# Optimization experiments

Hardware: AMD Instinct MI355X
Metric: run time of the kernel (lower is better)

## Reference

```python
import jax, jax.numpy as jnp
import numpy as np

N = 50000       # nodes
E = 800000      # edges (before self loops)
DIN = 128       # input feature width
H = 4           # heads
C = 64          # hidden width per head
NCLS = 2        # num classes
NEG_SLOPE = 0.2 # PyG GATConv default negative_slope


def setup_inputs() -> dict:
    key = jax.random.key(0)
    ks = jax.random.split(key, 16)
    x = jax.random.normal(ks[0], (N, DIN), dtype=jnp.float32)
    edge_index = jax.random.randint(ks[1], (2, E), 0, N, dtype=jnp.int64)
    s = 0.05
    # layer 0: DIN -> H*C
    W0 = jax.random.normal(ks[2], (DIN, H * C), dtype=jnp.float32) * s
    a_src0 = jax.random.normal(ks[3], (H, C), dtype=jnp.float32) * s
    a_dst0 = jax.random.normal(ks[4], (H, C), dtype=jnp.float32) * s
    b0 = jnp.zeros((H * C,), dtype=jnp.float32)
    # layer 1: H*C -> H*C
    W1 = jax.random.normal(ks[5], (H * C, H * C), dtype=jnp.float32) * s
    a_src1 = jax.random.normal(ks[6], (H, C), dtype=jnp.float32) * s
    a_dst1 = jax.random.normal(ks[7], (H, C), dtype=jnp.float32) * s
    b1 = jnp.zeros((H * C,), dtype=jnp.float32)
    # layer 2: H*C -> NCLS, single head
    W2 = jax.random.normal(ks[8], (H * C, NCLS), dtype=jnp.float32) * s
    a_src2 = jax.random.normal(ks[9], (1, NCLS), dtype=jnp.float32) * s
    a_dst2 = jax.random.normal(ks[10], (1, NCLS), dtype=jnp.float32) * s
    b2 = jnp.zeros((NCLS,), dtype=jnp.float32)
    return {"x": x, "edge_index": edge_index,
            "W0": W0, "a_src0": a_src0, "a_dst0": a_dst0, "b0": b0,
            "W1": W1, "a_src1": a_src1, "a_dst1": a_dst1, "b1": b1,
            "W2": W2, "a_src2": a_src2, "a_dst2": a_dst2, "b2": b2}


def gat_conv(x, ei, W, a_src, a_dst, b, heads, out_c):
    """PyG-style GATConv (add_self_loops already applied to ei, concat=True)."""
    n = x.shape[0]
    h = (x @ W).reshape(n, heads, out_c)              # [N, H, C]
    src, dst = ei[0], ei[1]
    asrc = (h * a_src).sum(-1)                         # [N, H]
    adst = (h * a_dst).sum(-1)                         # [N, H]
    alpha = jax.nn.leaky_relu(asrc[src] + adst[dst], NEG_SLOPE)  # [E', H]
    # segment softmax over incoming edges of each dst node
    amax = jax.ops.segment_max(alpha, dst, num_segments=n)        # [N, H]
    e = jnp.exp(alpha - amax[dst])
    denom = jax.ops.segment_sum(e, dst, num_segments=n)
    coef = e / denom[dst]                              # [E', H]
    msg = h[src] * coef[:, :, None]                    # [E', H, C]
    out = jax.ops.segment_sum(msg, dst, num_segments=n)           # [N, H, C]
    return out.reshape(n, heads * out_c) + b


def reference(x, edge_index, W0, a_src0, a_dst0, b0,
              W1, a_src1, a_dst1, b1, W2, a_src2, a_dst2, b2):
    # Inference mode: dropout(p=0.5, training=False) is identity.
    loops = jnp.arange(N, dtype=edge_index.dtype)
    ei = jnp.concatenate([edge_index, jnp.stack([loops, loops])], axis=1)
    h = jnp.tanh(gat_conv(x, ei, W0, a_src0, a_dst0, b0, H, C))
    h = jnp.tanh(gat_conv(h, ei, W1, a_src1, a_dst1, b1, H, C))
    h = gat_conv(h, ei, W2, a_src2, a_dst2, b2, 1, NCLS)
    return jax.nn.softmax(h, axis=1), h
```

## Files before the change

### kernel.cpp

```cpp
#include <hip/hip_runtime.h>

#define NEG 0.2f

typedef float f32x4 __attribute__((ext_vector_type(4)));
typedef short bf16x8 __attribute__((ext_vector_type(8)));

struct __align__(8) us4 { unsigned short v[4]; };
struct __align__(16) us8 { unsigned short v[8]; };

__device__ __forceinline__ float b2f(unsigned short u){
  union { unsigned int i; float f; } x; x.i = ((unsigned int)u) << 16; return x.f;
}
__device__ __forceinline__ unsigned short f2b(float f){
  union { float f; unsigned int i; } x; x.f = f;
  unsigned int r = x.i + 0x7FFFu + ((x.i >> 16) & 1u);
  return (unsigned short)(r >> 16);
}


__global__ void k_pack_w(const float* __restrict__ W, unsigned short* __restrict__ Wp, int K){
  int t = blockIdx.x*blockDim.x + threadIdx.x;
  int KB = K >> 5;
  if (t >= 16*KB*64) return;
  int lane = t & 63;
  int nb = (t >> 6) & 15;
  int kb = (t >> 6) >> 4;
  int kbase = kb*32 + ((lane>>4)<<3);
  int col = nb*16 + (lane&15);
  #pragma unroll
  for (int j=0;j<8;j++) Wp[(size_t)t*8 + j] = f2b(W[(size_t)(kbase+j)*256 + col]);
}

__global__ void k_detect(const int* __restrict__ ei, int* __restrict__ meta){
  if (blockIdx.x==0 && threadIdx.x==0){
    int o = 0;
    #pragma unroll
    for (int j=1;j<128;j+=2) o |= ei[j];
    meta[0] = (o==0) ? 1 : 0;
  }
}

__global__ void k_deg(const int* __restrict__ ei, const int* __restrict__ meta,
                      int* __restrict__ deg, int E, int EP, int N){
  int e = blockIdx.x*blockDim.x + threadIdx.x;
  if (e >= EP) return;
  int s, d;
  if (e < E){
    if (meta[0]){ s = ei[2*(size_t)e]; d = ei[2*(size_t)(E+e)]; }
    else        { s = ei[e];           d = ei[E+e]; }
  } else { s = d = e - E; }
  if ((unsigned)d >= (unsigned)N || (unsigned)s >= (unsigned)N) return;
  atomicAdd(deg + d, 1);
}

__global__ void k_scan1(const int* __restrict__ deg, int* __restrict__ tmp,
                        int* __restrict__ bsum, int N){
  __shared__ int s[256];
  int t = threadIdx.x;
  int i = blockIdx.x*256 + t;
  int v = (i < N) ? deg[i] : 0;
  s[t] = v;
  __syncthreads();
  for (int off=1; off<256; off<<=1){
    int x = (t>=off) ? s[t-off] : 0;
    __syncthreads();
    s[t] += x;
    __syncthreads();
  }
  if (i < N) tmp[i] = s[t] - v;
  if (t == 255) bsum[blockIdx.x] = s[255];
}

__global__ void k_scan2(const int* __restrict__ bsum, int* __restrict__ bsumx,
                        int* __restrict__ meta, int n){
  __shared__ int s[256];
  int t = threadIdx.x;
  int v = (t < n) ? bsum[t] : 0;
  s[t] = v;
  __syncthreads();
  for (int off=1; off<256; off<<=1){
    int x = (t>=off) ? s[t-off] : 0;
    __syncthreads();
    s[t] += x;
    __syncthreads();
  }
  bsumx[t] = s[t] - v;
  if (t == 255) meta[1] = s[255];
}

__global__ void k_scan3(const int* __restrict__ tmp, const int* __restrict__ bsumx,
                        const int* __restrict__ meta,
                        int* __restrict__ rp, int* __restrict__ cur, int N){
  int i = blockIdx.x*256 + threadIdx.x;
  if (i < N){ int v = tmp[i] + bsumx[i>>8]; rp[i] = v; cur[i] = v; }
  if (i == 0) rp[N] = meta[1];
}

__global__ void k_fill(const int* __restrict__ ei, const int* __restrict__ meta,
                       int* __restrict__ cur, int* __restrict__ csr, int E, int EP, int N){
  int e = blockIdx.x*blockDim.x + threadIdx.x;
  if (e >= EP) return;
  int s, d;
  if (e < E){
    if (meta[0]){ s = ei[2*(size_t)e]; d = ei[2*(size_t)(E+e)]; }
    else        { s = ei[e];           d = ei[E+e]; }
  } else { s = d = e - E; }
  if ((unsigned)d >= (unsigned)N || (unsigned)s >= (unsigned)N) return;
  int pos = atomicAdd(cur + d, 1);
  csr[pos] = s;
}

template<int K, int CVT>
__global__ __launch_bounds__(256) void k_gemm(const void* __restrict__ Xv,
    const unsigned short* __restrict__ Wp,
    const float* __restrict__ aS, const float* __restrict__ aD,
    unsigned short* __restrict__ Hout,
    float* __restrict__ asrc, float* __restrict__ adst, int N){
  constexpr int KB = K/32;
  __shared__ short sB[2][16*64*8];
  const int lane = threadIdx.x & 63;
  const int wave = threadIdx.x >> 6;
  const int rowbase = blockIdx.x*64 + wave*16;
  const int l15 = lane & 15, lhi = lane >> 4;
  const int arow = rowbase + l15;

  bf16x8 aF[KB];
  if (CVT){
    const float* X = (const float*)Xv;
    #pragma unroll
    for (int kb=0; kb<KB; kb++){
      bf16x8 a = {};
      if (arow < N){
        f32x4 v0 = *(const f32x4*)(X + (size_t)arow*K + kb*32 + lhi*8);
        f32x4 v1 = *(const f32x4*)(X + (size_t)arow*K + kb*32 + lhi*8 + 4);
        #pragma unroll
        for (int j=0;j<4;j++){ a[j] = (short)f2b(v0[j]); a[j+4] = (short)f2b(v1[j]); }
      }
      aF[kb] = a;
    }
  } else {
    const unsigned short* X = (const unsigned short*)Xv;
    #pragma unroll
    for (int kb=0; kb<KB; kb++){
      bf16x8 a = {};
      if (arow < N) a = *(const bf16x8*)(X + (size_t)arow*K + kb*32 + lhi*8);
      aF[kb] = a;
    }
  }

  auto stage = [&](int buf, int kb){
    #pragma unroll
    for (int q=0;q<4;q++){
      int nb = wave*4 + q;
      const unsigned short* gsrc = Wp + ((size_t)((kb*16 + nb)*64) + lane)*8;
      __builtin_amdgcn_global_load_lds(
          (const __attribute__((address_space(1))) void*)gsrc,
          (__attribute__((address_space(3))) void*)&sB[buf][(size_t)nb*64*8],
          16, 0, 0);
    }
  };

  f32x4 acc[16] = {};
  stage(0, 0);
  __syncthreads();
  #pragma unroll
  for (int kb=0; kb<KB; kb++){
    const int cur = kb & 1;
    if (kb+1 < KB) stage(cur^1, kb+1);
    #pragma unroll
    for (int nb=0; nb<16; nb++){
      bf16x8 b = *(const bf16x8*)(&sB[cur][((size_t)nb*64 + lane)*8]);
      acc[nb] = __builtin_amdgcn_mfma_f32_16x16x32_bf16(aF[kb], b, acc[nb], 0, 0, 0);
    }
    __syncthreads();
  }

  const int r0 = rowbase + lhi*4;

  float sp[4][4] = {}; float dp[4][4] = {};
  #pragma unroll
  for (int h=0; h<4; h++){
    #pragma unroll
    for (int q=0; q<4; q++){
      const int nb = h*4 + q;
      float ws = aS[h*64 + q*16 + l15];
      float wd = aD[h*64 + q*16 + l15];
      #pragma unroll
      for (int r=0;r<4;r++){ sp[r][h] += acc[nb][r]*ws; dp[r][h] += acc[nb][r]*wd; }
    }
  }
  #pragma unroll
  for (int m=1;m<16;m<<=1){
    #pragma unroll
    for (int r=0;r<4;r++){
      #pragma unroll
      for (int h=0;h<4;h++){
        sp[r][h] += __shfl_xor(sp[r][h], m);
        dp[r][h] += __shfl_xor(dp[r][h], m);
      }
    }
  }
  if (l15 < 4){
    const int h = l15;
    #pragma unroll
    for (int r=0;r<4;r++){
      int row = r0 + r;
      if (row < N){ asrc[row*4+h] = sp[r][h]; adst[row*4+h] = dp[r][h]; }
    }
  }
  #pragma unroll
  for (int nb=0;nb<16;nb++){
    #pragma unroll
    for (int r=0;r<4;r++){
      int row = r0 + r;
      if (row < N) Hout[(size_t)row*256 + nb*16 + l15] = f2b(acc[nb][r]);
    }
  }
}

__global__ __launch_bounds__(256) void k_agg(const unsigned short* __restrict__ Hb,
    const float* __restrict__ asrc, const float* __restrict__ adst,
    const int* __restrict__ rp, const int* __restrict__ csr,
    const float* __restrict__ bias, unsigned short* __restrict__ Xout, int N){
  const int lane = threadIdx.x & 63;
  const int dst = blockIdx.x*4 + (threadIdx.x >> 6);
  if (dst >= N) return;
  const int head = lane >> 4;
  const int c0 = lane*4;
  const float ad = adst[dst*4 + head];
  const int s0 = rp[dst], s1 = rp[dst+1];
  float a0=0.f,a1=0.f,a2=0.f,a3=0.f,den=0.f;
  int e = s0;
  for (; e+4 <= s1; e += 4){
    int i0 = csr[e+0], i1 = csr[e+1], i2 = csr[e+2], i3 = csr[e+3];
    float x0 = asrc[(size_t)i0*4 + head];
    float x1 = asrc[(size_t)i1*4 + head];
    float x2 = asrc[(size_t)i2*4 + head];
    float x3 = asrc[(size_t)i3*4 + head];
    us4 h0 = *(const us4*)(Hb + (size_t)i0*256 + c0);
    us4 h1 = *(const us4*)(Hb + (size_t)i1*256 + c0);
    us4 h2 = *(const us4*)(Hb + (size_t)i2*256 + c0);
    us4 h3 = *(const us4*)(Hb + (size_t)i3*256 + c0);
    x0 += ad; x0 = x0 > 0.f ? x0 : NEG*x0; float e0 = __expf(x0);
    x1 += ad; x1 = x1 > 0.f ? x1 : NEG*x1; float e1 = __expf(x1);
    x2 += ad; x2 = x2 > 0.f ? x2 : NEG*x2; float e2 = __expf(x2);
    x3 += ad; x3 = x3 > 0.f ? x3 : NEG*x3; float e3 = __expf(x3);
    den += (e0 + e1) + (e2 + e3);
    a0 += e0*b2f(h0.v[0]) + e1*b2f(h1.v[0]) + e2*b2f(h2.v[0]) + e3*b2f(h3.v[0]);
    a1 += e0*b2f(h0.v[1]) + e1*b2f(h1.v[1]) + e2*b2f(h2.v[1]) + e3*b2f(h3.v[1]);
    a2 += e0*b2f(h0.v[2]) + e1*b2f(h1.v[2]) + e2*b2f(h2.v[2]) + e3*b2f(h3.v[2]);
    a3 += e0*b2f(h0.v[3]) + e1*b2f(h1.v[3]) + e2*b2f(h2.v[3]) + e3*b2f(h3.v[3]);
  }
  for (; e < s1; e++){
    int src = csr[e];
    float al = asrc[(size_t)src*4 + head] + ad;
    al = al > 0.f ? al : NEG*al;
    float ee = __expf(al);
    den += ee;
    us4 hv = *(const us4*)(Hb + (size_t)src*256 + c0);
    a0 += ee * b2f(hv.v[0]);
    a1 += ee * b2f(hv.v[1]);
    a2 += ee * b2f(hv.v[2]);
    a3 += ee * b2f(hv.v[3]);
  }
  float rd = 1.0f/den;
  us4 o;
  o.v[0] = f2b(tanhf(a0*rd + bias[c0+0]));
  o.v[1] = f2b(tanhf(a1*rd + bias[c0+1]));
  o.v[2] = f2b(tanhf(a2*rd + bias[c0+2]));
  o.v[3] = f2b(tanhf(a3*rd + bias[c0+3]));
  *(us4*)(Xout + (size_t)dst*256 + c0) = o;
}

__global__ __launch_bounds__(256) void k_gemm2(const unsigned short* __restrict__ X,
    const float* __restrict__ W2, const float* __restrict__ as2, const float* __restrict__ ad2,
    float* __restrict__ H2, float* __restrict__ asrc2, float* __restrict__ adst2, int N){
  __shared__ float sW[512];
  const int t = threadIdx.x;
  sW[t] = W2[t]; sW[t+256] = W2[t+256];
  __syncthreads();
  const int row = blockIdx.x*16 + (t>>4);
  const int sub = t & 15;
  float a0=0.f, a1=0.f;
  if (row < N){
    const unsigned short* xp = X + (size_t)row*256 + sub*16;
    #pragma unroll
    for (int jj=0;jj<4;jj++){
      us4 hv = *(const us4*)(xp + jj*4);
      #pragma unroll
      for (int j=0;j<4;j++){
        float f = b2f(hv.v[j]);
        int k = sub*16 + jj*4 + j;
        a0 += f * sW[k*2+0];
        a1 += f * sW[k*2+1];
      }
    }
  }
  #pragma unroll
  for (int m=1;m<16;m<<=1){ a0 += __shfl_xor(a0,m); a1 += __shfl_xor(a1,m); }
  if (sub==0 && row<N){
    H2[row*2+0]=a0; H2[row*2+1]=a1;
    asrc2[row] = a0*as2[0] + a1*as2[1];
    adst2[row] = a0*ad2[0] + a1*ad2[1];
  }
}

__global__ __launch_bounds__(256) void k_agg2(const float* __restrict__ H2,
    const float* __restrict__ asrc2, const float* __restrict__ adst2,
    const int* __restrict__ rp, const int* __restrict__ csr, const float* __restrict__ bb,
    float* __restrict__ out, int N){
  const int lane = threadIdx.x & 63;
  const int dst = blockIdx.x*4 + (threadIdx.x >> 6);
  if (dst >= N) return;
  const float ad = adst2[dst];
  const int s0 = rp[dst], s1 = rp[dst+1];
  float n0=0.f, n1=0.f, den=0.f;
  for (int e=s0+lane; e<s1; e+=64){
    int src = csr[e];
    float al = asrc2[src] + ad;
    al = al>0.f ? al : NEG*al;
    float ee = __expf(al);
    den += ee;
    n0 += ee * H2[src*2+0];
    n1 += ee * H2[src*2+1];
  }
  #pragma unroll
  for (int m=1;m<64;m<<=1){
    n0 += __shfl_xor(n0,m); n1 += __shfl_xor(n1,m); den += __shfl_xor(den,m);
  }
  if (lane==0){
    float o0 = n0/den + bb[0];
    float o1 = n1/den + bb[1];
    float mx = fmaxf(o0,o1);
    float e0 = __expf(o0-mx), e1 = __expf(o1-mx);
    float is = 1.0f/(e0+e1);
    out[(size_t)dst*2+0] = e0*is;
    out[(size_t)dst*2+1] = e1*is;
    out[(size_t)2*N + dst*2+0] = o0;
    out[(size_t)2*N + dst*2+1] = o1;
  }
}

extern "C" void kernel_launch(void* const* d_in, const int* in_sizes, int n_in,
                              void* d_out, int out_size, void* d_ws, size_t ws_size,
                              hipStream_t stream){
  const float* x  = (const float*)d_in[0];
  const int*   ei = (const int*)d_in[1];
  const float* W0 = (const float*)d_in[2];
  const float* as0= (const float*)d_in[3];
  const float* ad0= (const float*)d_in[4];
  const float* b0 = (const float*)d_in[5];
  const float* W1 = (const float*)d_in[6];
  const float* as1= (const float*)d_in[7];
  const float* ad1= (const float*)d_in[8];
  const float* b1 = (const float*)d_in[9];
  const float* W2 = (const float*)d_in[10];
  const float* as2= (const float*)d_in[11];
  const float* ad2= (const float*)d_in[12];
  const float* b2 = (const float*)d_in[13];

  const int N  = in_sizes[0] / 128;
  const int E  = in_sizes[1] / 2;
  const int EP = E + N;
  float* outp = (float*)d_out;

  char* w = (char*)d_ws;
  size_t off = 0;
  auto alloc = [&](size_t bytes)->char*{
    char* p = w + off; off = (off + bytes + 255) & ~(size_t)255; return p;
  };
  unsigned short* hb  = (unsigned short*)alloc((size_t)N*256*2);
  unsigned short* xa  = (unsigned short*)alloc((size_t)N*256*2);
  float* asrc  = (float*)alloc((size_t)N*4*4);
  float* adst  = (float*)alloc((size_t)N*4*4);
  float* asrc2 = (float*)alloc((size_t)N*4);
  float* adst2 = (float*)alloc((size_t)N*4);
  float* H2    = (float*)alloc((size_t)N*2*4);
  unsigned short* Wp0 = (unsigned short*)alloc((size_t)128*256*2);
  unsigned short* Wp1 = (unsigned short*)alloc((size_t)256*256*2);
  int* deg   = (int*)alloc((size_t)N*4);
  int* rp    = (int*)alloc((size_t)(N+1)*4);
  int* cur   = (int*)alloc((size_t)N*4);
  int* tmp   = (int*)alloc((size_t)N*4);
  int* bsum  = (int*)alloc(256*4);
  int* bsumx = (int*)alloc(256*4);
  int* meta  = (int*)alloc(8*4);
  int* csr   = (int*)alloc((size_t)EP*4);
  (void)ws_size; (void)n_in; (void)out_size;

  hipMemsetAsync(deg, 0, (size_t)N*4, stream);

  k_pack_w<<<(16*(128/32)*64 + 255)/256, 256, 0, stream>>>(W0, Wp0, 128);
  k_pack_w<<<(16*(256/32)*64 + 255)/256, 256, 0, stream>>>(W1, Wp1, 256);
  k_detect<<<1, 64, 0, stream>>>(ei, meta);
  k_deg   <<<(EP + 255)/256, 256, 0, stream>>>(ei, meta, deg, E, EP, N);
  const int nb1 = (N + 255)/256;
  k_scan1 <<<nb1, 256, 0, stream>>>(deg, tmp, bsum, N);
  k_scan2 <<<1, 256, 0, stream>>>(bsum, bsumx, meta, nb1);
  k_scan3 <<<nb1, 256, 0, stream>>>(tmp, bsumx, meta, rp, cur, N);
  k_fill  <<<(EP + 255)/256, 256, 0, stream>>>(ei, meta, cur, csr, E, EP, N);

  k_gemm<128,1><<<(N + 63)/64, 256, 0, stream>>>(x, Wp0, as0, ad0, hb, asrc, adst, N);
  k_agg        <<<(N + 3)/4, 256, 0, stream>>>(hb, asrc, adst, rp, csr, b0, xa, N);
  k_gemm<256,0><<<(N + 63)/64, 256, 0, stream>>>(xa, Wp1, as1, ad1, hb, asrc, adst, N);
  k_agg        <<<(N + 3)/4, 256, 0, stream>>>(hb, asrc, adst, rp, csr, b1, xa, N);
  k_gemm2      <<<(N + 15)/16, 256, 0, stream>>>(xa, W2, as2, ad2, H2, asrc2, adst2, N);
  k_agg2       <<<(N + 3)/4, 256, 0, stream>>>(H2, asrc2, adst2, rp, csr, b2, outp, N);
}
```

Measured before the change: 322.9 us.

## Merge setup launches, unroll aggregation by 8, use 16 lanes per node in agg2

Merges the memset and detect step into one init kernel and packs both weight matrices in a single launch, which cuts launch count. The main aggregation loop now handles 8 edges per step, putting more independent gathers in flight. The final aggregation gives each destination 16 lanes instead of a full 64-lane wavefront, since average degree is only about 17. The costs are higher register pressure in k_agg and slightly more complex code.

Result: faster. 311.6 us (-3.5%).

```diff
diff --git a/kernel.cpp b/kernel.cpp
--- a/kernel.cpp
+++ b/kernel.cpp
@@ -6,7 +6,6 @@
 typedef short bf16x8 __attribute__((ext_vector_type(8)));
 
 struct __align__(8) us4 { unsigned short v[4]; };
-struct __align__(16) us8 { unsigned short v[8]; };
 
 __device__ __forceinline__ float b2f(unsigned short u){
   union { unsigned int i; float f; } x; x.i = ((unsigned int)u) << 16; return x.f;
@@ -18,10 +17,15 @@
 }
 
 
-__global__ void k_pack_w(const float* __restrict__ W, unsigned short* __restrict__ Wp, int K){
+__global__ void k_pack_w2(const float* __restrict__ W0, unsigned short* __restrict__ Wp0,
+                          const float* __restrict__ W1, unsigned short* __restrict__ Wp1){
   int t = blockIdx.x*blockDim.x + threadIdx.x;
-  int KB = K >> 5;
-  if (t >= 16*KB*64) return;
+  const int T0 = 16*4*64;
+  const int T1 = 16*8*64;
+  const float* W; unsigned short* Wp;
+  if (t < T0){ W = W0; Wp = Wp0; }
+  else if (t < T0 + T1){ W = W1; Wp = Wp1; t -= T0; }
+  else return;
   int lane = t & 63;
   int nb = (t >> 6) & 15;
   int kb = (t >> 6) >> 4;
@@ -31,8 +35,11 @@
   for (int j=0;j<8;j++) Wp[(size_t)t*8 + j] = f2b(W[(size_t)(kbase+j)*256 + col]);
 }
 
-__global__ void k_detect(const int* __restrict__ ei, int* __restrict__ meta){
-  if (blockIdx.x==0 && threadIdx.x==0){
+__global__ void k_init(const int* __restrict__ ei, int* __restrict__ meta,
+                       int* __restrict__ deg, int N){
+  int i = blockIdx.x*blockDim.x + threadIdx.x;
+  if (i < N) deg[i] = 0;
+  if (i == 0){
     int o = 0;
     #pragma unroll
     for (int j=1;j<128;j+=2) o |= ei[j];
@@ -231,6 +238,43 @@
   const int s0 = rp[dst], s1 = rp[dst+1];
   float a0=0.f,a1=0.f,a2=0.f,a3=0.f,den=0.f;
   int e = s0;
+  for (; e+8 <= s1; e += 8){
+    int i0 = csr[e+0], i1 = csr[e+1], i2 = csr[e+2], i3 = csr[e+3];
+    int i4 = csr[e+4], i5 = csr[e+5], i6 = csr[e+6], i7 = csr[e+7];
+    float x0 = asrc[(size_t)i0*4 + head];
+    float x1 = asrc[(size_t)i1*4 + head];
+    float x2 = asrc[(size_t)i2*4 + head];
+    float x3 = asrc[(size_t)i3*4 + head];
+    float x4 = asrc[(size_t)i4*4 + head];
+    float x5 = asrc[(size_t)i5*4 + head];
+    float x6 = asrc[(size_t)i6*4 + head];
+    float x7 = asrc[(size_t)i7*4 + head];
+    us4 h0 = *(const us4*)(Hb + (size_t)i0*256 + c0);
+    us4 h1 = *(const us4*)(Hb + (size_t)i1*256 + c0);
+    us4 h2 = *(const us4*)(Hb + (size_t)i2*256 + c0);
+    us4 h3 = *(const us4*)(Hb + (size_t)i3*256 + c0);
+    us4 h4 = *(const us4*)(Hb + (size_t)i4*256 + c0);
+    us4 h5 = *(const us4*)(Hb + (size_t)i5*256 + c0);
+    us4 h6 = *(const us4*)(Hb + (size_t)i6*256 + c0);
+    us4 h7 = *(const us4*)(Hb + (size_t)i7*256 + c0);
+    x0 += ad; x0 = x0 > 0.f ? x0 : NEG*x0; float e0 = __expf(x0);
+    x1 += ad; x1 = x1 > 0.f ? x1 : NEG*x1; float e1 = __expf(x1);
+    x2 += ad; x2 = x2 > 0.f ? x2 : NEG*x2; float e2 = __expf(x2);
+    x3 += ad; x3 = x3 > 0.f ? x3 : NEG*x3; float e3 = __expf(x3);
+    x4 += ad; x4 = x4 > 0.f ? x4 : NEG*x4; float e4 = __expf(x4);
+    x5 += ad; x5 = x5 > 0.f ? x5 : NEG*x5; float e5 = __expf(x5);
+    x6 += ad; x6 = x6 > 0.f ? x6 : NEG*x6; float e6 = __expf(x6);
+    x7 += ad; x7 = x7 > 0.f ? x7 : NEG*x7; float e7 = __expf(x7);
+    den += ((e0+e1)+(e2+e3)) + ((e4+e5)+(e6+e7));
+    a0 += e0*b2f(h0.v[0]) + e1*b2f(h1.v[0]) + e2*b2f(h2.v[0]) + e3*b2f(h3.v[0])
+        + e4*b2f(h4.v[0]) + e5*b2f(h5.v[0]) + e6*b2f(h6.v[0]) + e7*b2f(h7.v[0]);
+    a1 += e0*b2f(h0.v[1]) + e1*b2f(h1.v[1]) + e2*b2f(h2.v[1]) + e3*b2f(h3.v[1])
+        + e4*b2f(h4.v[1]) + e5*b2f(h5.v[1]) + e6*b2f(h6.v[1]) + e7*b2f(h7.v[1]);
+    a2 += e0*b2f(h0.v[2]) + e1*b2f(h1.v[2]) + e2*b2f(h2.v[2]) + e3*b2f(h3.v[2])
+        + e4*b2f(h4.v[2]) + e5*b2f(h5.v[2]) + e6*b2f(h6.v[2]) + e7*b2f(h7.v[2]);
+    a3 += e0*b2f(h0.v[3]) + e1*b2f(h1.v[3]) + e2*b2f(h2.v[3]) + e3*b2f(h3.v[3])
+        + e4*b2f(h4.v[3]) + e5*b2f(h5.v[3]) + e6*b2f(h6.v[3]) + e7*b2f(h7.v[3]);
+  }
   for (; e+4 <= s1; e += 4){
     int i0 = csr[e+0], i1 = csr[e+1], i2 = csr[e+2], i3 = csr[e+3];
     float x0 = asrc[(size_t)i0*4 + head];
@@ -309,13 +353,13 @@
     const float* __restrict__ asrc2, const float* __restrict__ adst2,
     const int* __restrict__ rp, const int* __restrict__ csr, const float* __restrict__ bb,
     float* __restrict__ out, int N){
-  const int lane = threadIdx.x & 63;
-  const int dst = blockIdx.x*4 + (threadIdx.x >> 6);
+  const int sub = threadIdx.x & 15;
+  const int dst = blockIdx.x*16 + (threadIdx.x >> 4);
   if (dst >= N) return;
   const float ad = adst2[dst];
   const int s0 = rp[dst], s1 = rp[dst+1];
   float n0=0.f, n1=0.f, den=0.f;
-  for (int e=s0+lane; e<s1; e+=64){
+  for (int e=s0+sub; e<s1; e+=16){
     int src = csr[e];
     float al = asrc2[src] + ad;
     al = al>0.f ? al : NEG*al;
@@ -325,10 +369,10 @@
     n1 += ee * H2[src*2+1];
   }
   #pragma unroll
-  for (int m=1;m<64;m<<=1){
+  for (int m=1;m<16;m<<=1){
     n0 += __shfl_xor(n0,m); n1 += __shfl_xor(n1,m); den += __shfl_xor(den,m);
   }
-  if (lane==0){
+  if (sub==0){
     float o0 = n0/den + bb[0];
     float o1 = n1/den + bb[1];
     float mx = fmaxf(o0,o1);
@@ -388,11 +432,8 @@
   int* csr   = (int*)alloc((size_t)EP*4);
   (void)ws_size; (void)n_in; (void)out_size;
 
-  hipMemsetAsync(deg, 0, (size_t)N*4, stream);
-
-  k_pack_w<<<(16*(128/32)*64 + 255)/256, 256, 0, stream>>>(W0, Wp0, 128);
-  k_pack_w<<<(16*(256/32)*64 + 255)/256, 256, 0, stream>>>(W1, Wp1, 256);
-  k_detect<<<1, 64, 0, stream>>>(ei, meta);
+  k_init  <<<(N + 255)/256, 256, 0, stream>>>(ei, meta, deg, N);
+  k_pack_w2<<<(16*4*64 + 16*8*64 + 255)/256, 256, 0, stream>>>(W0, Wp0, W1, Wp1);
   k_deg   <<<(EP + 255)/256, 256, 0, stream>>>(ei, meta, deg, E, EP, N);
   const int nb1 = (N + 255)/256;
   k_scan1 <<<nb1, 256, 0, stream>>>(deg, tmp, bsum, N);
@@ -405,5 +446,5 @@
   k_gemm<256,0><<<(N + 63)/64, 256, 0, stream>>>(xa, Wp1, as1, ad1, hb, asrc, adst, N);
   k_agg        <<<(N + 3)/4, 256, 0, stream>>>(hb, asrc, adst, rp, csr, b1, xa, N);
   k_gemm2      <<<(N + 15)/16, 256, 0, stream>>>(xa, W2, as2, ad2, H2, asrc2, adst2, N);
-  k_agg2       <<<(N + 3)/4, 256, 0, stream>>>(H2, asrc2, adst2, rp, csr, b2, outp, N);
-}
+  k_agg2       <<<(N + 15)/16, 256, 0, stream>>>(H2, asrc2, adst2, rp, csr, b2, outp, N);
+}
```
